# Optimization experiments

Hardware: AMD Instinct MI355X
Metric: run time of the kernel (lower is better)

## Reference

```python
import jax, jax.numpy as jnp
import numpy as np

B, N, D, H = 2, 2048, 768, 12
HD = D // H


def setup_inputs() -> dict:
    key = jax.random.key(0)
    ks = jax.random.split(key, 8)
    x = jax.random.normal(ks[0], (B, N, D), dtype=jnp.float32)
    dist = jax.random.randint(ks[1], (B, N, N), 0, 32, dtype=jnp.int32)
    mask = jax.random.bernoulli(ks[2], 0.1, (B, N))  # True = masked key
    # parameters (torch Linear stored pre-transposed: y = x @ W + b)
    s = 1.0 / np.sqrt(D)
    qkv_w = jax.random.uniform(ks[3], (D, 3 * D), jnp.float32, -s, s)
    qkv_b = jax.random.uniform(ks[4], (3 * D,), jnp.float32, -s, s)
    out_w = jax.random.uniform(ks[5], (D, D), jnp.float32, -s, s)
    out_b = jax.random.uniform(ks[6], (D,), jnp.float32, -s, s)
    bias_table = jax.random.normal(ks[7], (32, H), dtype=jnp.float32)
    return {"x": x, "dist": dist, "mask": mask, "qkv_w": qkv_w,
            "qkv_b": qkv_b, "out_w": out_w, "out_b": out_b,
            "bias_table": bias_table}


def reference(x, dist, mask, qkv_w, qkv_b, out_w, out_b, bias_table):
    scale = HD ** -0.5
    qkv = x @ qkv_w + qkv_b                      # [B,N,3D]
    q, k, v = jnp.split(qkv, 3, axis=-1)
    sh = lambda t: t.reshape(B, N, H, HD).transpose(0, 2, 1, 3)  # [B,H,N,HD]
    q, k, v = sh(q), sh(k), sh(v)
    a = jnp.einsum('bhnd,bhmd->bhnm', q, k) * scale  # [B,H,N,N]
    # relative-position bias: gather [B,N,N,H] -> [B,H,N,N]
    a = a + bias_table[jnp.clip(dist, 0, 31)].transpose(0, 3, 1, 2)
    a = jnp.where(mask[:, None, None, :], -jnp.inf, a)
    a = jax.nn.softmax(a.astype(jnp.float32), axis=-1)  # dropout: eval mode (p ignored)
    o = jnp.einsum('bhnm,bhmd->bhnd', a, v)            # [B,H,N,HD]
    o = o.transpose(0, 2, 1, 3).reshape(B, N, D)
    return o @ out_w + out_b
```

## Files before the change

kernel.cpp:

```cpp
#include <hip/hip_runtime.h>
#include <hip/hip_bf16.h>

typedef unsigned short u16;
typedef __attribute__((ext_vector_type(8))) short bf16x8;
typedef __attribute__((ext_vector_type(4))) short bf16x4;
typedef __attribute__((ext_vector_type(4))) float f32x4;

#define MFMA_BF16(a,b,c) __builtin_amdgcn_mfma_f32_16x16x32_bf16((a),(b),(c),0,0,0)
#define LOG2E 1.4426950408889634f

#if __has_builtin(__builtin_amdgcn_mfma_f32_16x16x16bf16_1k)
#define MFMA16(a,b,c) __builtin_amdgcn_mfma_f32_16x16x16bf16_1k((a),(b),(c),0,0,0)
#define HAVE_MFMA16 1
#elif __has_builtin(__builtin_amdgcn_mfma_f32_16x16x16_bf16)
#define MFMA16(a,b,c) __builtin_amdgcn_mfma_f32_16x16x16_bf16((a),(b),(c),0,0,0)
#define HAVE_MFMA16 1
#else
#define HAVE_MFMA16 0
#endif

__device__ __forceinline__ u16 f2b(float f) {
    __hip_bfloat16 h = __float2bfloat16(f);
    u16 u; __builtin_memcpy(&u, &h, 2); return u;
}
__device__ __forceinline__ f32x4 zero4() { f32x4 z = {0.f,0.f,0.f,0.f}; return z; }

__device__ __forceinline__ void gl_lds16(const u16* g, u16* l) {
    __builtin_amdgcn_global_load_lds(
        (const __attribute__((address_space(1))) unsigned int*)g,
        (__attribute__((address_space(3))) unsigned int*)l,
        16, 0, 0);
}

__global__ __launch_bounds__(256) void convX(const float* __restrict__ in, u16* __restrict__ out) {
    size_t i = ((size_t)blockIdx.x * 256 + threadIdx.x) * 8;
    float4 a = *(const float4*)(in + i);
    float4 b = *(const float4*)(in + i + 4);
    union { u16 s[8]; uint4 v; } u;
    u.s[0]=f2b(a.x); u.s[1]=f2b(a.y); u.s[2]=f2b(a.z); u.s[3]=f2b(a.w);
    u.s[4]=f2b(b.x); u.s[5]=f2b(b.y); u.s[6]=f2b(b.z); u.s[7]=f2b(b.w);
    *(uint4*)(out + i) = u.v;
}

__global__ __launch_bounds__(256) void packDist(const int* __restrict__ din,
                                                const unsigned long long* __restrict__ mbits,
                                                unsigned char* __restrict__ dout) {
    size_t i = ((size_t)blockIdx.x * 256 + threadIdx.x) * 4;
    int4 v = *(const int4*)(din + i);
    int b = (int)(i >> 22);
    int j = (int)(i & 2047);
    unsigned bits = (unsigned)((mbits[b*32 + (j >> 6)] >> (j & 63)) & 0xFull);
    uchar4 o;
    o.x = (bits & 1u) ? 32 : (unsigned char)min(max(v.x, 0), 31);
    o.y = (bits & 2u) ? 32 : (unsigned char)min(max(v.y, 0), 31);
    o.z = (bits & 4u) ? 32 : (unsigned char)min(max(v.z, 0), 31);
    o.w = (bits & 8u) ? 32 : (unsigned char)min(max(v.w, 0), 31);
    *(uchar4*)(dout + i) = o;
}

__global__ __launch_bounds__(256) void convTW(const float* __restrict__ in, u16* __restrict__ out, int C) {
    __shared__ __align__(16) u16 T[64][68];
    int c0 = blockIdx.x * 64, k0 = blockIdx.y * 64;
    int tid = threadIdx.x;
#pragma unroll
    for (int i = 0; i < 4; ++i) {
        int id = tid + i * 256;
        int row = id >> 4, ch = id & 15;
        float4 v = *(const float4*)(in + (size_t)(k0 + row) * C + c0 + ch * 4);
        T[row][ch*4+0] = f2b(v.x); T[row][ch*4+1] = f2b(v.y);
        T[row][ch*4+2] = f2b(v.z); T[row][ch*4+3] = f2b(v.w);
    }
    __syncthreads();
#pragma unroll
    for (int i = 0; i < 2; ++i) {
        int id = tid + i * 256;
        int c = id >> 3, ch = id & 7;
        union { u16 s[8]; uint4 v; } u;
#pragma unroll
        for (int j = 0; j < 8; ++j) u.s[j] = T[ch*8+j][c];
        *(uint4*)(out + (size_t)(c0 + c) * 768 + k0 + ch * 8) = u.v;
    }
}

__global__ void detectMaskBits(const unsigned* __restrict__ m, unsigned long long* __restrict__ mbits) {
    __shared__ int sB, sH, sF;
    if (threadIdx.x == 0) { sB = 0; sH = 0; sF = 0; }
    __syncthreads();
    int lb = 0, lh = 0, lf = 0;
#pragma unroll
    for (int i = 0; i < 4; ++i) {
        unsigned v = m[threadIdx.x + i * 256];
        if (v == 0x3f800000u) { lf = 1; }
        else if (v > 1u) {
            unsigned b0 = v & 0xffu, b1 = (v >> 8) & 0xffu, b2 = (v >> 16) & 0xffu, b3 = v >> 24;
            bool bytesOK = (b0 <= 1u) && (b1 <= 1u) && (b2 <= 1u) && (b3 <= 1u);
            unsigned h0 = v & 0xffffu, h1 = v >> 16;
            bool halfOK = (h0 == 0u || h0 == 0x3f80u) && (h1 == 0u || h1 == 0x3f80u);
            if (bytesOK) lb = 1; else if (halfOK) lh = 1;
        }
    }
    if (lb) atomicOr(&sB, 1);
    if (lh) atomicOr(&sH, 1);
    if (lf) atomicOr(&sF, 1);
    __syncthreads();
    int mode = sH ? 3 : (sB ? 1 : (sF ? 2 : 0));
    const unsigned char* m8 = (const unsigned char*)m;
    const u16* mh = (const u16*)m;
    const float* mf = (const float*)m;
    const int* mi = (const int*)m;
    for (int it = 0; it < 16; ++it) {
        int e = it * 256 + threadIdx.x;
        int pred;
        if (mode == 0)      pred = (mi[e] != 0);
        else if (mode == 1) pred = (m8[e] != 0);
        else if (mode == 2) pred = (mf[e] != 0.0f);
        else                pred = (mh[e] != 0);
        unsigned long long bal = __ballot(pred);
        if ((threadIdx.x & 63) == 0) mbits[it * 4 + (threadIdx.x >> 6)] = bal;
    }
}

template<int MODE>
__global__ __launch_bounds__(256)
void gemmBT(const u16* __restrict__ A, const u16* __restrict__ Bt,
            const float* __restrict__ bias,
            u16* __restrict__ qO, u16* __restrict__ kO, u16* __restrict__ vO,
            float* __restrict__ fO) {
    __shared__ __align__(16) u16 As[2][128*32];
    __shared__ __align__(16) u16 Bs[2][128*32];
    const int K = 768;
    const int tid = threadIdx.x;
    const int lane = tid & 63, w = tid >> 6;
    const int wm = w >> 1, wn = w & 1;
    const int l15 = lane & 15, q = lane >> 4;
    const int m0 = blockIdx.y * 128, n0 = blockIdx.x * 128;
    const int stRow = (lane >> 2);
    const int stChunk = (lane & 3) ^ ((lane >> 3) & 3);
    const u16* Ag = A + (size_t)(m0 + w*32 + stRow) * K + stChunk * 8;
    const u16* Bg = Bt + (size_t)(n0 + w*32 + stRow) * K + stChunk * 8;
    u16* ldsA = &As[0][0] + w*32*32;
    u16* ldsB = &Bs[0][0] + w*32*32;
    const int fA = (q ^ ((l15 >> 1) & 3)) * 8;

    f32x4 acc[4][4];
#pragma unroll
    for (int i=0;i<4;++i)
#pragma unroll
        for (int j=0;j<4;++j) acc[i][j] = zero4();

#pragma unroll
    for (int c = 0; c < 2; ++c) {
        gl_lds16(Ag + (size_t)(c*16) * K, ldsA + c*16*32);
        gl_lds16(Bg + (size_t)(c*16) * K, ldsB + c*16*32);
    }
    __syncthreads();

    int cur = 0;
    for (int kt = 0; kt < 24; ++kt) {
        if (kt < 23) {
            const int ko = (kt + 1) * 32;
            u16* dA = &As[cur^1][0] + w*32*32;
            u16* dB = &Bs[cur^1][0] + w*32*32;
#pragma unroll
            for (int c = 0; c < 2; ++c) {
                gl_lds16(Ag + (size_t)(c*16) * K + ko, dA + c*16*32);
                gl_lds16(Bg + (size_t)(c*16) * K + ko, dB + c*16*32);
            }
        }
        const u16* as = &As[cur][0];
        const u16* bs = &Bs[cur][0];
        bf16x8 af[4], bfr[4];
#pragma unroll
        for (int mt=0; mt<4; ++mt) af[mt]  = *(const bf16x8*)(as + (wm*64+mt*16+l15)*32 + fA);
#pragma unroll
        for (int nt=0; nt<4; ++nt) bfr[nt] = *(const bf16x8*)(bs + (wn*64+nt*16+l15)*32 + fA);
#pragma unroll
        for (int mt=0; mt<4; ++mt)
#pragma unroll
            for (int nt=0; nt<4; ++nt)
                acc[mt][nt] = MFMA_BF16(af[mt], bfr[nt], acc[mt][nt]);
        __syncthreads();
        cur ^= 1;
    }

#pragma unroll
    for (int mt=0; mt<4; ++mt) {
#pragma unroll
        for (int nt=0; nt<4; ++nt) {
            int n = n0 + wn*64 + nt*16 + l15;
            float bv = bias[n];
            if (MODE == 0) {
                int which = n / 768;
                int rem = n - which*768;
                int hh = rem >> 6, hd = rem & 63;
                int mBase = m0 + wm*64 + mt*16 + q*4;
                int b = mBase >> 11, tok0 = mBase & 2047;
                if (which == 2) {
                    union { u16 s4[4]; unsigned long long u; } pv;
#pragma unroll
                    for (int r=0; r<4; ++r) pv.s4[r] = f2b(acc[mt][nt][r] + bv);
                    *(unsigned long long*)(vO + ((size_t)(b*12 + hh)*64 + hd)*2048 + tok0) = pv.u;
                } else {
#pragma unroll
                    for (int r=0; r<4; ++r) {
                        float v = acc[mt][nt][r] + bv;
                        size_t di = (((size_t)(b*12 + hh))*2048 + tok0 + r)*64 + hd;
                        if (which == 0) qO[di] = f2b(v * (0.125f * LOG2E));
                        else            kO[di] = f2b(v);
                    }
                }
            } else {
#pragma unroll
                for (int r=0; r<4; ++r) {
                    int m = m0 + wm*64 + mt*16 + q*4 + r;
                    fO[(size_t)m*768 + n] = acc[mt][nt][r] + bv;
                }
            }
        }
    }
}

__global__ __launch_bounds__(256)
void flashAttn(const u16* __restrict__ Qb, const u16* __restrict__ Kb,
               const u16* __restrict__ Vt, const unsigned char* __restrict__ dist8,
               const float* __restrict__ btg, u16* __restrict__ attnout) {
    __shared__ float bt[33];
    __shared__ __align__(16) u16 KT[2][4096];
    __shared__ __align__(16) u16 VT[2][4096];
    __shared__ __align__(16) u16 Os[4][16][72];
    const int tid = threadIdx.x;
    const int lane = tid & 63, w = tid >> 6;
    const int l15 = lane & 15, q = lane >> 4;
    const int wg = blockIdx.x + 32 * (blockIdx.y + 12 * blockIdx.z);
    const int xcd = wg & 7, slot = wg >> 3;
    const int g = ((slot >> 5) << 3) + xcd;
    const int i0 = (slot & 31) * 64;
    const int b = g / 12, h = g - b * 12;
    const int bh = g;
    const float NEG_INF = -__builtin_inff();
    if (tid < 33) bt[tid] = (tid == 32) ? NEG_INF : btg[tid*12 + h] * LOG2E;

    const int iRow = i0 + w*16 + l15;
    const u16* Qp = Qb + ((size_t)bh*2048 + iRow)*64;
    bf16x8 qB0 = *(const bf16x8*)(Qp + q*8);
    bf16x8 qB1 = *(const bf16x8*)(Qp + 32 + q*8);
    const unsigned char* dp = dist8 + ((size_t)(b*2048 + iRow))*2048 + q*4;
#if !HAVE_MFMA16
    const int srcL0 = ((2*q)   & 3)*16 + l15;
    const int srcL1 = ((2*q+1) & 3)*16 + l15;
    union { unsigned u4[4]; bf16x8 v; } one_;
    { unsigned oc = (l15 == 0) ? 0x3F803F80u : 0u;
      one_.u4[0]=oc; one_.u4[1]=oc; one_.u4[2]=oc; one_.u4[3]=oc; }
#else
    union { unsigned u2[2]; bf16x4 v; } one4_;
    { unsigned oc = (l15 == 0) ? 0x3F803F80u : 0u;
      one4_.u2[0]=oc; one4_.u2[1]=oc; }
#endif

    const int stRow = w*16 + (lane >> 3);
    const int stCol = (((lane & 7) ^ (lane >> 3)) << 4);
    const char* kgB = (const char*)Kb + (size_t)bh*2048*128;
    const char* vgB = (const char*)Vt + (size_t)bh*64*4096;
    const int swz = (l15 & 7) << 4;
    const int f0 = (q*16)      ^ swz;
    const int f1 = (q*16 + 64) ^ swz;
    const int rB = l15 * 128;

    {
        u16* kd = &KT[0][0] + w*1024;
        u16* vd = &VT[0][0] + w*1024;
#pragma unroll
        for (int c = 0; c < 2; ++c) {
            int row = stRow + c*8;
            gl_lds16((const u16*)(kgB + (size_t)row*128 + stCol),  kd + c*512);
            gl_lds16((const u16*)(vgB + (size_t)row*4096 + stCol), vd + c*512);
        }
    }
    __syncthreads();

    f32x4 o0 = zero4(), o1 = zero4(), o2 = zero4(), o3 = zero4(), o4 = zero4();
    float mI = NEG_INF;
    int cur = 0;

    for (int jt = 0; jt < 32; ++jt) {
        const int j0 = jt * 64;
        if (jt < 31) {
            const int j0n = j0 + 64;
            u16* kd = &KT[cur^1][0] + w*1024;
            u16* vd = &VT[cur^1][0] + w*1024;
#pragma unroll
            for (int c = 0; c < 2; ++c) {
                int row = stRow + c*8;
                gl_lds16((const u16*)(kgB + (size_t)(j0n + row)*128 + stCol),          kd + c*512);
                gl_lds16((const u16*)(vgB + (size_t)row*4096 + (size_t)j0n*2 + stCol), vd + c*512);
            }
        }
        unsigned dv4[4];
#pragma unroll
        for (int mt = 0; mt < 4; ++mt) dv4[mt] = *(const unsigned*)(dp + j0 + mt*16);

        const char* kt = (const char*)&KT[cur][0];
        f32x4 s0 = zero4(), s1 = zero4(), s2 = zero4(), s3 = zero4();
        {
            bf16x8 k00 = *(const bf16x8*)(kt + rB          + f0);
            bf16x8 k01 = *(const bf16x8*)(kt + rB          + f1);
            bf16x8 k10 = *(const bf16x8*)(kt + rB + 2048   + f0);
            bf16x8 k11 = *(const bf16x8*)(kt + rB + 2048   + f1);
            bf16x8 k20 = *(const bf16x8*)(kt + rB + 4096   + f0);
            bf16x8 k21 = *(const bf16x8*)(kt + rB + 4096   + f1);
            bf16x8 k30 = *(const bf16x8*)(kt + rB + 6144   + f0);
            bf16x8 k31 = *(const bf16x8*)(kt + rB + 6144   + f1);
            __builtin_amdgcn_s_setprio(1);
            s0 = MFMA_BF16(k00, qB0, s0); s0 = MFMA_BF16(k01, qB1, s0);
            s1 = MFMA_BF16(k10, qB0, s1); s1 = MFMA_BF16(k11, qB1, s1);
            s2 = MFMA_BF16(k20, qB0, s2); s2 = MFMA_BF16(k21, qB1, s2);
            s3 = MFMA_BF16(k30, qB0, s3); s3 = MFMA_BF16(k31, qB1, s3);
            __builtin_amdgcn_s_setprio(0);
        }

        float sv[4][4];
#pragma unroll
        for (int mt = 0; mt < 4; ++mt) {
            const f32x4 sm = mt==0 ? s0 : (mt==1 ? s1 : (mt==2 ? s2 : s3));
            const unsigned d4 = dv4[mt];
#pragma unroll
            for (int r = 0; r < 4; ++r) {
                int dd = (d4 >> (r*8)) & 255;
                sv[mt][r] = sm[r] + bt[dd];
            }
        }

        float t0 = fmaxf(fmaxf(sv[0][0], sv[0][1]), fmaxf(sv[0][2], sv[0][3]));
        float t1 = fmaxf(fmaxf(sv[1][0], sv[1][1]), fmaxf(sv[1][2], sv[1][3]));
        float t2 = fmaxf(fmaxf(sv[2][0], sv[2][1]), fmaxf(sv[2][2], sv[2][3]));
        float t3 = fmaxf(fmaxf(sv[3][0], sv[3][1]), fmaxf(sv[3][2], sv[3][3]));
        float rm = fmaxf(fmaxf(t0, t1), fmaxf(t2, t3));
        rm = fmaxf(rm, __shfl_xor(rm, 16, 64));
        rm = fmaxf(rm, __shfl_xor(rm, 32, 64));
        if (!__all(rm <= mI)) {
            float mn = fmaxf(mI, rm);
            float al = exp2f(mI - mn);
            mI = mn;
#pragma unroll
            for (int r = 0; r < 4; ++r) { o0[r] *= al; o1[r] *= al; o2[r] *= al; o3[r] *= al; }
            o4[0] *= al;
        }
        float p[4][4];
#pragma unroll
        for (int mt = 0; mt < 4; ++mt)
#pragma unroll
            for (int r = 0; r < 4; ++r) p[mt][r] = exp2f(sv[mt][r] - mI);

        const char* vt = (const char*)&VT[cur][0];
#if HAVE_MFMA16
        __builtin_amdgcn_s_setprio(1);
#pragma unroll
        for (int mt = 0; mt < 4; ++mt) {
            union { unsigned d[2]; bf16x4 v; } pu;
            pu.d[0] = (unsigned)f2b(p[mt][0]) | ((unsigned)f2b(p[mt][1]) << 16);
            pu.d[1] = (unsigned)f2b(p[mt][2]) | ((unsigned)f2b(p[mt][3]) << 16);
            const int cbase = (((mt*2 + (q>>1)) ^ (l15 & 7)) << 4) + (q & 1)*8;
            bf16x4 v0 = *(const bf16x4*)(vt + rB          + cbase);
            bf16x4 v1 = *(const bf16x4*)(vt + rB + 2048   + cbase);
            bf16x4 v2 = *(const bf16x4*)(vt + rB + 4096   + cbase);
            bf16x4 v3 = *(const bf16x4*)(vt + rB + 6144   + cbase);
            o0 = MFMA16(v0, pu.v, o0);
            o1 = MFMA16(v1, pu.v, o1);
            o2 = MFMA16(v2, pu.v, o2);
            o3 = MFMA16(v3, pu.v, o3);
            o4 = MFMA16(one4_.v, pu.v, o4);
        }
        __builtin_amdgcn_s_setprio(0);
#else
        unsigned pk[4][2];
#pragma unroll
        for (int mt = 0; mt < 4; ++mt) {
            pk[mt][0] = (unsigned)f2b(p[mt][0]) | ((unsigned)f2b(p[mt][1]) << 16);
            pk[mt][1] = (unsigned)f2b(p[mt][2]) | ((unsigned)f2b(p[mt][3]) << 16);
        }
        __builtin_amdgcn_s_setprio(1);
#pragma unroll
        for (int ks = 0; ks < 2; ++ks) {
            union { unsigned d[4]; bf16x8 v; } pb;
#pragma unroll
            for (int s = 0; s < 4; ++s) {
                int sl = (s >> 1) ? srcL1 : srcL0;
                int u0 = __shfl((int)pk[2*ks    ][s & 1], sl, 64);
                int u1 = __shfl((int)pk[2*ks + 1][s & 1], sl, 64);
                pb.d[s] = (q >> 1) ? (unsigned)u1 : (unsigned)u0;
            }
            const int fk = ks ? f1 : f0;
            bf16x8 v0 = *(const bf16x8*)(vt + rB          + fk);
            bf16x8 v1 = *(const bf16x8*)(vt + rB + 2048   + fk);
            bf16x8 v2 = *(const bf16x8*)(vt + rB + 4096   + fk);
            bf16x8 v3 = *(const bf16x8*)(vt + rB + 6144   + fk);
            o0 = MFMA_BF16(v0, pb.v, o0);
            o1 = MFMA_BF16(v1, pb.v, o1);
            o2 = MFMA_BF16(v2, pb.v, o2);
            o3 = MFMA_BF16(v3, pb.v, o3);
            o4 = MFMA_BF16(one_.v, pb.v, o4);
        }
        __builtin_amdgcn_s_setprio(0);
#endif

        __syncthreads();
        cur ^= 1;
    }

    float lsum = __shfl(o4[0], l15, 64);
    float inv = 1.0f / lsum;
#pragma unroll
    for (int r = 0; r < 4; ++r) {
        Os[w][l15][ 0 + q*4 + r] = f2b(o0[r] * inv);
        Os[w][l15][16 + q*4 + r] = f2b(o1[r] * inv);
        Os[w][l15][32 + q*4 + r] = f2b(o2[r] * inv);
        Os[w][l15][48 + q*4 + r] = f2b(o3[r] * inv);
    }
    __syncthreads();
    int rr = lane >> 2, cc = lane & 3;
    uint4 a0 = *(const uint4*)&Os[w][rr][cc*16];
    uint4 a1 = *(const uint4*)&Os[w][rr][cc*16 + 8];
    size_t orow = ((size_t)b*2048 + i0 + w*16 + rr)*768 + h*64 + cc*16;
    *(uint4*)(attnout + orow)     = a0;
    *(uint4*)(attnout + orow + 8) = a1;
}

extern "C" void kernel_launch(void* const* d_in, const int* in_sizes, int n_in,
                              void* d_out, int out_size, void* d_ws, size_t ws_size,
                              hipStream_t stream) {
    (void)in_sizes; (void)n_in; (void)out_size; (void)ws_size;
    const float* x      = (const float*)d_in[0];
    const int*   dist   = (const int*)d_in[1];
    const int*   mask   = (const int*)d_in[2];
    const float* qkv_w  = (const float*)d_in[3];
    const float* qkv_b  = (const float*)d_in[4];
    const float* out_w  = (const float*)d_in[5];
    const float* out_b  = (const float*)d_in[6];
    const float* btab   = (const float*)d_in[7];
    float* out = (float*)d_out;

    char* ws = (char*)d_ws;
    size_t off = 0;
    auto alloc = [&](size_t bytes) { void* p = ws + off; off += (bytes + 255) & ~(size_t)255; return p; };
    u16* xb      = (u16*)alloc((size_t)4096*768*2);
    u16* wqkvT   = (u16*)alloc((size_t)2304*768*2);
    u16* woutT   = (u16*)alloc((size_t)768*768*2);
    u16* Qb      = (u16*)alloc((size_t)24*2048*64*2);
    u16* Kb      = (u16*)alloc((size_t)24*2048*64*2);
    u16* Vtp     = (u16*)alloc((size_t)24*2048*64*2);
    u16* attnout = (u16*)alloc((size_t)4096*768*2);
    unsigned char* dist8 = (unsigned char*)alloc((size_t)2*2048*2048);
    unsigned long long* mbits = (unsigned long long*)alloc(64*8);

    convX<<<1536, 256, 0, stream>>>(x, xb);
    detectMaskBits<<<1, 256, 0, stream>>>((const unsigned*)mask, mbits);
    packDist<<<8192, 256, 0, stream>>>(dist, mbits, dist8);
    convTW<<<dim3(36,12), 256, 0, stream>>>(qkv_w, wqkvT, 2304);
    convTW<<<dim3(12,12), 256, 0, stream>>>(out_w, woutT, 768);
    gemmBT<0><<<dim3(18,32), 256, 0, stream>>>(xb, wqkvT, qkv_b, Qb, Kb, Vtp, nullptr);
    flashAttn<<<dim3(32,12,2), 256, 0, stream>>>(Qb, Kb, Vtp, dist8, btab, attnout);
    gemmBT<1><<<dim3(6,32), 256, 0, stream>>>(attnout, woutT, out_b, nullptr, nullptr, nullptr, out);
}
```

Baseline: 254.2 us.

## Fuse prep kernels, stage dist tiles via LDS, add smaller-tile output GEMM

```diff
diff --git a/kernel.cpp b/kernel.cpp
--- a/kernel.cpp
+++ b/kernel.cpp
@@ -32,91 +32,98 @@
         16, 0, 0);
 }
 
-__global__ __launch_bounds__(256) void convX(const float* __restrict__ in, u16* __restrict__ out) {
-    size_t i = ((size_t)blockIdx.x * 256 + threadIdx.x) * 8;
-    float4 a = *(const float4*)(in + i);
-    float4 b = *(const float4*)(in + i + 4);
-    union { u16 s[8]; uint4 v; } u;
-    u.s[0]=f2b(a.x); u.s[1]=f2b(a.y); u.s[2]=f2b(a.z); u.s[3]=f2b(a.w);
-    u.s[4]=f2b(b.x); u.s[5]=f2b(b.y); u.s[6]=f2b(b.z); u.s[7]=f2b(b.w);
-    *(uint4*)(out + i) = u.v;
-}
-
-__global__ __launch_bounds__(256) void packDist(const int* __restrict__ din,
-                                                const unsigned long long* __restrict__ mbits,
-                                                unsigned char* __restrict__ dout) {
-    size_t i = ((size_t)blockIdx.x * 256 + threadIdx.x) * 4;
-    int4 v = *(const int4*)(din + i);
-    int b = (int)(i >> 22);
-    int j = (int)(i & 2047);
-    unsigned bits = (unsigned)((mbits[b*32 + (j >> 6)] >> (j & 63)) & 0xFull);
-    uchar4 o;
-    o.x = (bits & 1u) ? 32 : (unsigned char)min(max(v.x, 0), 31);
-    o.y = (bits & 2u) ? 32 : (unsigned char)min(max(v.y, 0), 31);
-    o.z = (bits & 4u) ? 32 : (unsigned char)min(max(v.z, 0), 31);
-    o.w = (bits & 8u) ? 32 : (unsigned char)min(max(v.w, 0), 31);
-    *(uchar4*)(dout + i) = o;
-}
-
-__global__ __launch_bounds__(256) void convTW(const float* __restrict__ in, u16* __restrict__ out, int C) {
+__global__ __launch_bounds__(256)
+void prep(const float* __restrict__ x, u16* __restrict__ xb,
+          const float* __restrict__ qkv_w, u16* __restrict__ wqkvT,
+          const float* __restrict__ out_w, u16* __restrict__ woutT,
+          const int* __restrict__ dist, const unsigned* __restrict__ mask,
+          unsigned char* __restrict__ dist8) {
     __shared__ __align__(16) u16 T[64][68];
-    int c0 = blockIdx.x * 64, k0 = blockIdx.y * 64;
-    int tid = threadIdx.x;
-#pragma unroll
-    for (int i = 0; i < 4; ++i) {
-        int id = tid + i * 256;
-        int row = id >> 4, ch = id & 15;
-        float4 v = *(const float4*)(in + (size_t)(k0 + row) * C + c0 + ch * 4);
-        T[row][ch*4+0] = f2b(v.x); T[row][ch*4+1] = f2b(v.y);
-        T[row][ch*4+2] = f2b(v.z); T[row][ch*4+3] = f2b(v.w);
-    }
-    __syncthreads();
-#pragma unroll
-    for (int i = 0; i < 2; ++i) {
-        int id = tid + i * 256;
-        int c = id >> 3, ch = id & 7;
+    __shared__ int sB, sH, sF;
+    const int bid = blockIdx.x;
+    const int tid = threadIdx.x;
+    if (bid < 8192) {
+        if (tid == 0) { sB = 0; sH = 0; sF = 0; }
+        __syncthreads();
+        int lb = 0, lh = 0, lf = 0;
+#pragma unroll
+        for (int i = 0; i < 4; ++i) {
+            unsigned v = mask[tid + i * 256];
+            if (v == 0x3f800000u) { lf = 1; }
+            else if (v > 1u) {
+                unsigned b0 = v & 0xffu, b1 = (v >> 8) & 0xffu, b2 = (v >> 16) & 0xffu, b3 = v >> 24;
+                bool bytesOK = (b0 <= 1u) && (b1 <= 1u) && (b2 <= 1u) && (b3 <= 1u);
+                unsigned h0 = v & 0xffffu, h1 = v >> 16;
+                bool halfOK = (h0 == 0u || h0 == 0x3f80u) && (h1 == 0u || h1 == 0x3f80u);
+                if (bytesOK) lb = 1; else if (halfOK) lh = 1;
+            }
+        }
+        if (lb) atomicOr(&sB, 1);
+        if (lh) atomicOr(&sH, 1);
+        if (lf) atomicOr(&sF, 1);
+        __syncthreads();
+        int mode = sH ? 3 : (sB ? 1 : (sF ? 2 : 0));
+        size_t i = ((size_t)bid * 256 + tid) * 4;
+        int4 v = *(const int4*)(dist + i);
+        int b = (int)(i >> 22), j = (int)(i & 2047);
+        int base = b * 2048 + j;
+        int mk0, mk1, mk2, mk3;
+        if (mode == 0) {
+            int4 mv = *(const int4*)((const int*)mask + base);
+            mk0 = mv.x != 0; mk1 = mv.y != 0; mk2 = mv.z != 0; mk3 = mv.w != 0;
+        } else if (mode == 1) {
+            const unsigned char* m8 = (const unsigned char*)mask;
+            mk0 = m8[base] != 0; mk1 = m8[base+1] != 0; mk2 = m8[base+2] != 0; mk3 = m8[base+3] != 0;
+        } else if (mode == 2) {
+            float4 mv = *(const float4*)((const float*)mask + base);
+            mk0 = mv.x != 0.f; mk1 = mv.y != 0.f; mk2 = mv.z != 0.f; mk3 = mv.w != 0.f;
+        } else {
+            const u16* mh = (const u16*)mask;
+            mk0 = mh[base] != 0; mk1 = mh[base+1] != 0; mk2 = mh[base+2] != 0; mk3 = mh[base+3] != 0;
+        }
+        uchar4 o;
+        o.x = mk0 ? 32 : (unsigned char)min(max(v.x, 0), 31);
+        o.y = mk1 ? 32 : (unsigned char)min(max(v.y, 0), 31);
+        o.z = mk2 ? 32 : (unsigned char)min(max(v.z, 0), 31);
+        o.w = mk3 ? 32 : (unsigned char)min(max(v.w, 0), 31);
+        *(uchar4*)(dist8 + i) = o;
+    } else if (bid < 8192 + 1536) {
+        size_t i = ((size_t)(bid - 8192) * 256 + tid) * 8;
+        float4 a = *(const float4*)(x + i);
+        float4 b = *(const float4*)(x + i + 4);
         union { u16 s[8]; uint4 v; } u;
-#pragma unroll
-        for (int j = 0; j < 8; ++j) u.s[j] = T[ch*8+j][c];
-        *(uint4*)(out + (size_t)(c0 + c) * 768 + k0 + ch * 8) = u.v;
-    }
-}
-
-__global__ void detectMaskBits(const unsigned* __restrict__ m, unsigned long long* __restrict__ mbits) {
-    __shared__ int sB, sH, sF;
-    if (threadIdx.x == 0) { sB = 0; sH = 0; sF = 0; }
-    __syncthreads();
-    int lb = 0, lh = 0, lf = 0;
-#pragma unroll
-    for (int i = 0; i < 4; ++i) {
-        unsigned v = m[threadIdx.x + i * 256];
-        if (v == 0x3f800000u) { lf = 1; }
-        else if (v > 1u) {
-            unsigned b0 = v & 0xffu, b1 = (v >> 8) & 0xffu, b2 = (v >> 16) & 0xffu, b3 = v >> 24;
-            bool bytesOK = (b0 <= 1u) && (b1 <= 1u) && (b2 <= 1u) && (b3 <= 1u);
-            unsigned h0 = v & 0xffffu, h1 = v >> 16;
-            bool halfOK = (h0 == 0u || h0 == 0x3f80u) && (h1 == 0u || h1 == 0x3f80u);
-            if (bytesOK) lb = 1; else if (halfOK) lh = 1;
-        }
-    }
-    if (lb) atomicOr(&sB, 1);
-    if (lh) atomicOr(&sH, 1);
-    if (lf) atomicOr(&sF, 1);
-    __syncthreads();
-    int mode = sH ? 3 : (sB ? 1 : (sF ? 2 : 0));
-    const unsigned char* m8 = (const unsigned char*)m;
-    const u16* mh = (const u16*)m;
-    const float* mf = (const float*)m;
-    const int* mi = (const int*)m;
-    for (int it = 0; it < 16; ++it) {
-        int e = it * 256 + threadIdx.x;
-        int pred;
-        if (mode == 0)      pred = (mi[e] != 0);
-        else if (mode == 1) pred = (m8[e] != 0);
-        else if (mode == 2) pred = (mf[e] != 0.0f);
-        else                pred = (mh[e] != 0);
-        unsigned long long bal = __ballot(pred);
-        if ((threadIdx.x & 63) == 0) mbits[it * 4 + (threadIdx.x >> 6)] = bal;
+        u.s[0]=f2b(a.x); u.s[1]=f2b(a.y); u.s[2]=f2b(a.z); u.s[3]=f2b(a.w);
+        u.s[4]=f2b(b.x); u.s[5]=f2b(b.y); u.s[6]=f2b(b.z); u.s[7]=f2b(b.w);
+        *(uint4*)(xb + i) = u.v;
+    } else {
+        const float* in; u16* out; int C, c0, k0;
+        if (bid < 8192 + 1536 + 432) {
+            int s = bid - (8192 + 1536);
+            in = qkv_w; out = wqkvT; C = 2304;
+            c0 = (s % 36) * 64; k0 = (s / 36) * 64;
+        } else {
+            int s = bid - (8192 + 1536 + 432);
+            in = out_w; out = woutT; C = 768;
+            c0 = (s % 12) * 64; k0 = (s / 12) * 64;
+        }
+#pragma unroll
+        for (int i = 0; i < 4; ++i) {
+            int id = tid + i * 256;
+            int row = id >> 4, ch = id & 15;
+            float4 v = *(const float4*)(in + (size_t)(k0 + row) * C + c0 + ch * 4);
+            T[row][ch*4+0] = f2b(v.x); T[row][ch*4+1] = f2b(v.y);
+            T[row][ch*4+2] = f2b(v.z); T[row][ch*4+3] = f2b(v.w);
+        }
+        __syncthreads();
+#pragma unroll
+        for (int i = 0; i < 2; ++i) {
+            int id = tid + i * 256;
+            int c = id >> 3, ch = id & 7;
+            union { u16 s[8]; uint4 v; } u;
+#pragma unroll
+            for (int jj = 0; jj < 8; ++jj) u.s[jj] = T[ch*8+jj][c];
+            *(uint4*)(out + (size_t)(c0 + c) * 768 + k0 + ch * 8) = u.v;
+        }
     }
 }
 
@@ -221,12 +228,68 @@
 }
 
 __global__ __launch_bounds__(256)
+void gemmOut(const u16* __restrict__ A, const u16* __restrict__ Bt,
+             const float* __restrict__ bias, float* __restrict__ fO) {
+    __shared__ __align__(16) u16 As[2][64*32];
+    __shared__ __align__(16) u16 Bs[2][64*32];
+    const int K = 768;
+    const int tid = threadIdx.x;
+    const int lane = tid & 63, w = tid >> 6;
+    const int l15 = lane & 15, q = lane >> 4;
+    const int m0 = blockIdx.y * 64, n0 = blockIdx.x * 64;
+    const int stRow = tid >> 2;
+    const int stChunk = (tid & 3) ^ ((tid >> 3) & 3);
+    const u16* Ag = A + (size_t)(m0 + stRow) * K + stChunk * 8;
+    const u16* Bg = Bt + (size_t)(n0 + stRow) * K + stChunk * 8;
+    const int fA = (q ^ ((l15 >> 1) & 3)) * 8;
+
+    f32x4 acc[4];
+#pragma unroll
+    for (int i=0;i<4;++i) acc[i] = zero4();
+
+    gl_lds16(Ag, &As[0][0] + w*512);
+    gl_lds16(Bg, &Bs[0][0] + w*512);
+    __syncthreads();
+
+    int cur = 0;
+    for (int kt = 0; kt < 24; ++kt) {
+        if (kt < 23) {
+            const int ko = (kt + 1) * 32;
+            gl_lds16(Ag + ko, &As[cur^1][0] + w*512);
+            gl_lds16(Bg + ko, &Bs[cur^1][0] + w*512);
+        }
+        const u16* as = &As[cur][0];
+        const u16* bs = &Bs[cur][0];
+        bf16x8 af = *(const bf16x8*)(as + (w*16 + l15)*32 + fA);
+        bf16x8 bfr[4];
+#pragma unroll
+        for (int nt=0; nt<4; ++nt) bfr[nt] = *(const bf16x8*)(bs + (nt*16+l15)*32 + fA);
+#pragma unroll
+        for (int nt=0; nt<4; ++nt) acc[nt] = MFMA_BF16(af, bfr[nt], acc[nt]);
+        __syncthreads();
+        cur ^= 1;
+    }
+
+#pragma unroll
+    for (int nt=0; nt<4; ++nt) {
+        int n = n0 + nt*16 + l15;
+        float bv = bias[n];
+#pragma unroll
+        for (int r=0; r<4; ++r) {
+            int m = m0 + w*16 + q*4 + r;
+            fO[(size_t)m*768 + n] = acc[nt][r] + bv;
+        }
+    }
+}
+
+__global__ __launch_bounds__(256)
 void flashAttn(const u16* __restrict__ Qb, const u16* __restrict__ Kb,
                const u16* __restrict__ Vt, const unsigned char* __restrict__ dist8,
                const float* __restrict__ btg, u16* __restrict__ attnout) {
     __shared__ float bt[33];
     __shared__ __align__(16) u16 KT[2][4096];
     __shared__ __align__(16) u16 VT[2][4096];
+    __shared__ __align__(16) u16 DT[2][2048];
     __shared__ __align__(16) u16 Os[4][16][72];
     const int tid = threadIdx.x;
     const int lane = tid & 63, w = tid >> 6;
@@ -244,7 +307,6 @@
     const u16* Qp = Qb + ((size_t)bh*2048 + iRow)*64;
     bf16x8 qB0 = *(const bf16x8*)(Qp + q*8);
     bf16x8 qB1 = *(const bf16x8*)(Qp + 32 + q*8);
-    const unsigned char* dp = dist8 + ((size_t)(b*2048 + iRow))*2048 + q*4;
 #if !HAVE_MFMA16
     const int srcL0 = ((2*q)   & 3)*16 + l15;
     const int srcL1 = ((2*q+1) & 3)*16 + l15;
@@ -259,12 +321,17 @@
 
     const int stRow = w*16 + (lane >> 3);
     const int stCol = (((lane & 7) ^ (lane >> 3)) << 4);
+    const int dRow = w*16 + (lane >> 2);
+    const int dCol = ((lane & 3) ^ ((lane >> 3) & 3)) << 4;
     const char* kgB = (const char*)Kb + (size_t)bh*2048*128;
     const char* vgB = (const char*)Vt + (size_t)bh*64*4096;
+    const unsigned char* dgB = dist8 + (size_t)(b*2048 + i0)*2048;
     const int swz = (l15 & 7) << 4;
     const int f0 = (q*16)      ^ swz;
     const int f1 = (q*16 + 64) ^ swz;
     const int rB = l15 * 128;
+    const int rD = (w*16 + l15) * 64;
+    const int dsw = (l15 >> 1) & 3;
 
     {
         u16* kd = &KT[0][0] + w*1024;
@@ -275,6 +342,8 @@
             gl_lds16((const u16*)(kgB + (size_t)row*128 + stCol),  kd + c*512);
             gl_lds16((const u16*)(vgB + (size_t)row*4096 + stCol), vd + c*512);
         }
+        gl_lds16((const u16*)(dgB + (size_t)dRow*2048 + dCol),
+                 (u16*)((char*)&DT[0][0] + w*1024));
     }
     __syncthreads();
 
@@ -294,10 +363,14 @@
                 gl_lds16((const u16*)(kgB + (size_t)(j0n + row)*128 + stCol),          kd + c*512);
                 gl_lds16((const u16*)(vgB + (size_t)row*4096 + (size_t)j0n*2 + stCol), vd + c*512);
             }
-        }
+            gl_lds16((const u16*)(dgB + (size_t)dRow*2048 + j0n + dCol),
+                     (u16*)((char*)&DT[cur^1][0] + w*1024));
+        }
+        const char* dt = (const char*)&DT[cur][0];
         unsigned dv4[4];
 #pragma unroll
-        for (int mt = 0; mt < 4; ++mt) dv4[mt] = *(const unsigned*)(dp + j0 + mt*16);
+        for (int mt = 0; mt < 4; ++mt)
+            dv4[mt] = *(const unsigned*)(dt + rD + ((mt ^ dsw) << 4) + q*4);
 
         const char* kt = (const char*)&KT[cur][0];
         f32x4 s0 = zero4(), s1 = zero4(), s2 = zero4(), s3 = zero4();
@@ -450,14 +523,10 @@
     u16* Vtp     = (u16*)alloc((size_t)24*2048*64*2);
     u16* attnout = (u16*)alloc((size_t)4096*768*2);
     unsigned char* dist8 = (unsigned char*)alloc((size_t)2*2048*2048);
-    unsigned long long* mbits = (unsigned long long*)alloc(64*8);
-
-    convX<<<1536, 256, 0, stream>>>(x, xb);
-    detectMaskBits<<<1, 256, 0, stream>>>((const unsigned*)mask, mbits);
-    packDist<<<8192, 256, 0, stream>>>(dist, mbits, dist8);
-    convTW<<<dim3(36,12), 256, 0, stream>>>(qkv_w, wqkvT, 2304);
-    convTW<<<dim3(12,12), 256, 0, stream>>>(out_w, woutT, 768);
+
+    prep<<<8192 + 1536 + 432 + 144, 256, 0, stream>>>(
+        x, xb, qkv_w, wqkvT, out_w, woutT, dist, (const unsigned*)mask, dist8);
     gemmBT<0><<<dim3(18,32), 256, 0, stream>>>(xb, wqkvT, qkv_b, Qb, Kb, Vtp, nullptr);
     flashAttn<<<dim3(32,12,2), 256, 0, stream>>>(Qb, Kb, Vtp, dist8, btab, attnout);
-    gemmBT<1><<<dim3(6,32), 256, 0, stream>>>(attnout, woutT, out_b, nullptr, nullptr, nullptr, out);
-}
+    gemmOut<<<dim3(12,64), 256, 0, stream>>>(attnout, woutT, out_b, out);
+}
```

After: 227.6 us. 1.12x faster.
